# Optimization experiments

Measured on AMD Instinct MI355X. Metric: run time of the kernel, lower is better.

## Reference

```python
import jax, jax.numpy as jnp
import numpy as np

B, S, DIM, HEADS, DHEAD = 1, 1992, 2048, 16, 128
NKI_SEQ_ALIGN = 128
EPS = 1e-6


def setup_inputs() -> dict:
    key = jax.random.key(0)
    ks = jax.random.split(key, 8)
    hidden_states = jax.random.normal(ks[0], (B, S, DIM), dtype=jnp.float32)
    # realistic rotary tables, full head_dim with interleaved pair angles
    pos = jnp.arange(S, dtype=jnp.float32)
    inv_freq = 1.0 / (10000.0 ** (jnp.arange(0, DHEAD, 2, dtype=jnp.float32) / DHEAD))
    ang = pos[:, None] * inv_freq[None, :]                      # [S, DHEAD/2]
    full = jnp.stack([ang, ang], axis=-1).reshape(S, DHEAD)     # interleave
    freqs_cos = jnp.cos(full)[None, :, None, :]                 # [1,S,1,DHEAD]
    freqs_sin = jnp.sin(full)[None, :, None, :]
    sc = 0.02
    wq = jax.random.normal(ks[1], (DIM, DIM), dtype=jnp.float32) * sc
    wk = jax.random.normal(ks[2], (DIM, DIM), dtype=jnp.float32) * sc
    wv = jax.random.normal(ks[3], (DIM, DIM), dtype=jnp.float32) * sc
    wo = jax.random.normal(ks[4], (DIM, DIM), dtype=jnp.float32) * sc
    bq = jax.random.normal(ks[5], (DIM,), dtype=jnp.float32) * sc
    bk = jax.random.normal(ks[6], (DIM,), dtype=jnp.float32) * sc
    bv = jax.random.normal(ks[7], (DIM,), dtype=jnp.float32) * sc
    bo = jnp.zeros((DIM,), dtype=jnp.float32)
    norm_q_w = jnp.ones((DIM,), dtype=jnp.float32)
    norm_k_w = jnp.ones((DIM,), dtype=jnp.float32)
    return dict(hidden_states=hidden_states, freqs_cos=freqs_cos, freqs_sin=freqs_sin,
                wq=wq, bq=bq, wk=wk, bk=bk, wv=wv, bv=bv,
                norm_q_w=norm_q_w, norm_k_w=norm_k_w, wo=wo, bo=bo)


def _rms_norm(x, weight, eps=EPS):
    xf = x.astype(jnp.float32)
    var = jnp.mean(xf * xf, axis=-1, keepdims=True)
    return (weight * (xf * jax.lax.rsqrt(var + eps))).astype(x.dtype)


def _apply_rope(x, freqs_cos, freqs_sin):
    # x: [B,H,S,D]; freqs: [1,S,1,D]
    cos = jnp.transpose(freqs_cos[..., 0::2], (0, 2, 1, 3))  # [1,1,S,D/2]
    sin = jnp.transpose(freqs_sin[..., 1::2], (0, 2, 1, 3))
    x1, x2 = x[..., 0::2], x[..., 1::2]
    o1 = x1 * cos - x2 * sin
    o2 = x1 * sin + x2 * cos
    return jnp.stack([o1, o2], axis=-1).reshape(x.shape)


def _attention_padded(q, k, v):
    # Faithful to nki_flash_attention: zero-pad seq to multiple of 128,
    # no masking of padded keys (they contribute logit 0), trim query pad.
    B_, H_, S_, D_ = q.shape
    pad = (-S_) % NKI_SEQ_ALIGN
    if pad:
        pc = [(0, 0), (0, 0), (0, pad), (0, 0)]
        q = jnp.pad(q, pc); k = jnp.pad(k, pc); v = jnp.pad(v, pc)
    scale = 1.0 / np.sqrt(D_)
    scores = jnp.einsum('bhqd,bhkd->bhqk', q, k) * scale
    probs = jax.nn.softmax(scores, axis=-1)
    out = jnp.einsum('bhqk,bhkd->bhqd', probs, v)
    return out[:, :, :S_, :]


def reference(hidden_states, freqs_cos, freqs_sin, wq, bq, wk, bk, wv, bv,
              norm_q_w, norm_k_w, wo, bo):
    b, s, _ = hidden_states.shape
    q = hidden_states @ wq.T + bq
    k = hidden_states @ wk.T + bk
    v = hidden_states @ wv.T + bv
    q = _rms_norm(q, norm_q_w)
    k = _rms_norm(k, norm_k_w)
    hd = q.shape[-1] // HEADS
    q = q.reshape(b, s, HEADS, hd).transpose(0, 2, 1, 3)
    k = k.reshape(b, s, HEADS, hd).transpose(0, 2, 1, 3)
    v = v.reshape(b, s, HEADS, hd).transpose(0, 2, 1, 3)
    q = _apply_rope(q, freqs_cos, freqs_sin)
    k = _apply_rope(k, freqs_cos, freqs_sin)
    o = _attention_padded(q, k, v)
    o = o.transpose(0, 2, 1, 3).reshape(b, s, -1)
    return o @ wo.T + bo
```

## Files before the change

kernel.cpp:

```cpp
#include <hip/hip_runtime.h>
#include <cstdint>

#define S_REAL 1992
#define S_PAD  2048
#define DIMSZ  2048
#define NHEAD  16
#define DHD    128

typedef float f32x4 __attribute__((ext_vector_type(4)));
typedef __bf16 bf16x8 __attribute__((ext_vector_type(8)));
typedef unsigned short u16x8 __attribute__((ext_vector_type(8)));

__device__ __forceinline__ unsigned short f2bf(float f){
  uint32_t u = __float_as_uint(f);
  u += 0x7fffu + ((u >> 16) & 1u);
  return (unsigned short)(u >> 16);
}

__device__ __forceinline__ void gload16(const void* g, void* l){
  __builtin_amdgcn_global_load_lds(
      (const __attribute__((address_space(1))) uint32_t*)g,
      (__attribute__((address_space(3))) uint32_t*)l,
      16, 0, 0);
}

template<int N> __device__ __forceinline__ void waitbar(){
  if constexpr (N == 8)      asm volatile("s_waitcnt vmcnt(8)\n\ts_barrier" ::: "memory");
  else if constexpr (N == 6) asm volatile("s_waitcnt vmcnt(6)\n\ts_barrier" ::: "memory");
  else if constexpr (N == 4) asm volatile("s_waitcnt vmcnt(4)\n\ts_barrier" ::: "memory");
  else if constexpr (N == 3) asm volatile("s_waitcnt vmcnt(3)\n\ts_barrier" ::: "memory");
  else if constexpr (N == 2) asm volatile("s_waitcnt vmcnt(2)\n\ts_barrier" ::: "memory");
  else                       asm volatile("s_waitcnt vmcnt(0)\n\ts_barrier" ::: "memory");
}

__launch_bounds__(256)
__global__ void k_cvt(const float* __restrict__ src, unsigned short* __restrict__ dst, int n8){
  int i = blockIdx.x * 256 + threadIdx.x;
  if (i >= n8) return;
  const float4* s = (const float4*)src + (size_t)i * 2;
  float4 a = s[0], b = s[1];
  u16x8 o;
  o[0]=f2bf(a.x); o[1]=f2bf(a.y); o[2]=f2bf(a.z); o[3]=f2bf(a.w);
  o[4]=f2bf(b.x); o[5]=f2bf(b.y); o[6]=f2bf(b.z); o[7]=f2bf(b.w);
  *((u16x8*)dst + i) = o;
}

template<int BM, int BN>
__launch_bounds__(512, 2)
__global__ void k_gemm8(const unsigned short* __restrict__ A,
                        const unsigned short* __restrict__ B0,
                        const unsigned short* __restrict__ B1,
                        const unsigned short* __restrict__ B2,
                        const float* __restrict__ bias0,
                        const float* __restrict__ bias1,
                        const float* __restrict__ bias2,
                        float* __restrict__ C0, float* __restrict__ C1, float* __restrict__ C2,
                        int Mreal)
{
  constexpr int WN   = BN / 64;
  constexpr int WM   = 8 / WN;
  constexpr int RM   = BM / WM;
  constexpr int MI   = RM / 16;
  constexpr int NL   = (BM + BN) / 128;
  constexpr int BUFE = (BM + BN) * 32;
  constexpr int BOFF = BM * 32;
  constexpr int NT   = DIMSZ / 32;

  __shared__ unsigned short lds[4 * BUFE];

  const unsigned short* Bm = (blockIdx.z == 0) ? B0 : ((blockIdx.z == 1) ? B1 : B2);
  const float* bias        = (blockIdx.z == 0) ? bias0 : ((blockIdx.z == 1) ? bias1 : bias2);
  float* C                 = (blockIdx.z == 0) ? C0 : ((blockIdx.z == 1) ? C1 : C2);

  const int tid = threadIdx.x;
  const int w = tid >> 6, l = tid & 63;
  const int lr = l & 15, lg = l >> 4;
  const int m0 = blockIdx.x * BM, n0 = blockIdx.y * BN;
  const int wr = (w / WN) * RM, wc = (w % WN) * 64;

  f32x4 acc[MI][4];
  #pragma unroll
  for (int mi = 0; mi < MI; ++mi)
    #pragma unroll
    for (int ni = 0; ni < 4; ++ni)
      acc[mi][ni] = (f32x4){0.f, 0.f, 0.f, 0.f};

#define G8_STAGE(TT) do{                                                          \
    const int k0s = (TT) * 32;                                                    \
    unsigned short* dst = &lds[((TT) & 3) * BUFE];                                \
    _Pragma("unroll")                                                             \
    for (int i_ = 0; i_ < BM / 128; ++i_){                                        \
      int lin = i_ * 512 + tid;                                                   \
      int r_ = lin >> 2, pos_ = lin & 3;                                          \
      int gr_ = m0 + r_; if (gr_ > Mreal - 1) gr_ = Mreal - 1;                    \
      gload16(A + (size_t)gr_ * DIMSZ + k0s + (pos_ ^ ((r_ >> 1) & 3)) * 8,       \
              dst + lin * 8);                                                     \
    }                                                                             \
    _Pragma("unroll")                                                             \
    for (int i_ = 0; i_ < BN / 128; ++i_){                                        \
      int lin = i_ * 512 + tid;                                                   \
      int r_ = lin >> 2, pos_ = lin & 3;                                          \
      gload16(Bm + (size_t)(n0 + r_) * DIMSZ + k0s + (pos_ ^ ((r_ >> 1) & 3)) * 8,\
              dst + BOFF + lin * 8);                                              \
    }                                                                             \
  } while(0)

#define G8_COMPUTE(TT) do{                                                        \
    const unsigned short* sb = &lds[((TT) & 3) * BUFE];                           \
    bf16x8 af_[MI]; bf16x8 bf_[4];                                                \
    _Pragma("unroll")                                                             \
    for (int mi = 0; mi < MI; ++mi){                                              \
      int r_ = wr + mi * 16 + lr;                                                 \
      af_[mi] = *(const bf16x8*)(sb + r_ * 32 + (lg ^ ((r_ >> 1) & 3)) * 8);      \
    }                                                                             \
    _Pragma("unroll")                                                             \
    for (int ni = 0; ni < 4; ++ni){                                               \
      int r_ = wc + ni * 16 + lr;                                                 \
      bf_[ni] = *(const bf16x8*)(sb + BOFF + r_ * 32 + (lg ^ ((r_ >> 1) & 3)) * 8);\
    }                                                                             \
    __builtin_amdgcn_s_setprio(1);                                                \
    _Pragma("unroll")                                                             \
    for (int mi = 0; mi < MI; ++mi)                                               \
      _Pragma("unroll")                                                           \
      for (int ni = 0; ni < 4; ++ni)                                              \
        acc[mi][ni] = __builtin_amdgcn_mfma_f32_16x16x32_bf16(af_[mi], bf_[ni],   \
                                                              acc[mi][ni], 0, 0, 0);\
    __builtin_amdgcn_s_setprio(0);                                                \
  } while(0)

  G8_STAGE(0); G8_STAGE(1); G8_STAGE(2);

  for (int tt = 0; tt < NT - 3; ++tt){
    waitbar<2 * NL>();
    G8_STAGE(tt + 3);
    G8_COMPUTE(tt);
  }
  waitbar<2 * NL>(); G8_COMPUTE(NT - 3);
  waitbar<NL>();     G8_COMPUTE(NT - 2);
  waitbar<0>();      G8_COMPUTE(NT - 1);

#undef G8_STAGE
#undef G8_COMPUTE

  #pragma unroll
  for (int ni = 0; ni < 4; ++ni){
    int col = n0 + wc + ni * 16 + lr;
    float bz = bias[col];
    #pragma unroll
    for (int mi = 0; mi < MI; ++mi){
      #pragma unroll
      for (int j = 0; j < 4; ++j){
        int row = m0 + wr + mi * 16 + lg * 4 + j;
        if (row < Mreal) C[(size_t)row * DIMSZ + col] = acc[mi][ni][j] + bz;
      }
    }
  }
}

__launch_bounds__(256)
__global__ void k_normrope(const float* __restrict__ Xf, const float* __restrict__ nw,
                           const float* __restrict__ fc, const float* __restrict__ fs,
                           unsigned short* __restrict__ Out, float scale, int swz)
{
  const int s = blockIdx.x;
  const int t = threadIdx.x;
  const int w = t >> 6, l = t & 63;
  __shared__ float wred[4];
  float v[8];
  float ss = 0.f;
  if (s < S_REAL){
    const float4* p = (const float4*)(Xf + (size_t)s * DIMSZ) + t * 2;
    float4 a = p[0], b = p[1];
    v[0]=a.x; v[1]=a.y; v[2]=a.z; v[3]=a.w; v[4]=b.x; v[5]=b.y; v[6]=b.z; v[7]=b.w;
    #pragma unroll
    for (int j = 0; j < 8; ++j) ss += v[j] * v[j];
  }
  #pragma unroll
  for (int off = 32; off >= 1; off >>= 1) ss += __shfl_xor(ss, off);
  if (l == 0) wred[w] = ss;
  __syncthreads();
  float tot = wred[0] + wred[1] + wred[2] + wred[3];
  float rinv = rsqrtf(tot * (1.f / DIMSZ) + 1e-6f);

  const int h  = t >> 4;
  const int d0 = (t & 15) * 8;
  const int b  = t & 15;
  const int bsw = swz ? (b ^ (s & 7)) : b;
  unsigned short* dst = Out + ((size_t)h * S_PAD + s) * DHD + bsw * 8;
  u16x8 o;
  if (s < S_REAL){
    #pragma unroll
    for (int i = 0; i < 4; ++i){
      float c_ = fc[s * DHD + d0 + 2 * i];
      float s_ = fs[s * DHD + d0 + 2 * i + 1];
      float x1 = v[2 * i]     * rinv * nw[t * 8 + 2 * i];
      float x2 = v[2 * i + 1] * rinv * nw[t * 8 + 2 * i + 1];
      o[2 * i]     = f2bf((x1 * c_ - x2 * s_) * scale);
      o[2 * i + 1] = f2bf((x1 * s_ + x2 * c_) * scale);
    }
  } else {
    #pragma unroll
    for (int j = 0; j < 8; ++j) o[j] = 0;
  }
  *(u16x8*)dst = o;
}

__launch_bounds__(256)
__global__ void k_vtrans(const float* __restrict__ Vf, unsigned short* __restrict__ Vth)
{
  __shared__ unsigned short tile[64][72];
  const int t = threadIdx.x;
  const int s0 = blockIdx.x * 64, c0 = blockIdx.y * 64;
  #pragma unroll
  for (int i = 0; i < 4; ++i){
    int r = (t >> 4) * 4 + i;
    int s = s0 + r;
    int cq = (t & 15) * 4;
    float4 val = {0.f, 0.f, 0.f, 0.f};
    if (s < S_REAL) val = *((const float4*)(Vf + (size_t)s * DIMSZ + c0) + (t & 15));
    tile[r][cq + 0] = f2bf(val.x);
    tile[r][cq + 1] = f2bf(val.y);
    tile[r][cq + 2] = f2bf(val.z);
    tile[r][cq + 3] = f2bf(val.w);
  }
  __syncthreads();
  const int cl = t >> 2;
  const int cc = c0 + cl;
  #pragma unroll
  for (int bi = 0; bi < 2; ++bi){
    int b = (t & 3) * 2 + bi;
    u16x8 o;
    #pragma unroll
    for (int j = 0; j < 8; ++j) o[j] = tile[b * 8 + j][cl];
    int bsw = b ^ (cc & 7);
    *(u16x8*)(Vth + (size_t)cc * S_PAD + s0 + bsw * 8) = o;
  }
}

__launch_bounds__(256)
__global__ void k_attn(const unsigned short* __restrict__ Qh,
                       const unsigned short* __restrict__ Kh,
                       const unsigned short* __restrict__ Vth,
                       unsigned short* __restrict__ O)
{
  __shared__ unsigned short kbuf[2][64 * 128];
  __shared__ unsigned short vbuf[2][128 * 64];
  __shared__ unsigned short pbuf[4][16 * 64];
  const int h = blockIdx.y;
  const int q0 = blockIdx.x * 64;
  const int t = threadIdx.x, w = t >> 6, l = t & 63;
  const int lr = l & 15, lg = l >> 4;

  const unsigned short* Qp = Qh + ((size_t)h * S_PAD + q0 + w * 16 + lr) * DHD;
  bf16x8 qf[4];
  #pragma unroll
  for (int ks = 0; ks < 4; ++ks) qf[ks] = *(const bf16x8*)(Qp + ks * 32 + lg * 8);

  f32x4 acc[8];
  #pragma unroll
  for (int nf = 0; nf < 8; ++nf) acc[nf] = (f32x4){0.f, 0.f, 0.f, 0.f};
  float m = -3.0e38f, lsum = 0.f;

#define ATT_STAGE(KT, BI) do{                                                       \
    _Pragma("unroll")                                                               \
    for (int i_ = 0; i_ < 4; ++i_){                                                 \
      int rK = (w * 4 + i_) * 4 + (l >> 4);                                         \
      gload16(Kh + ((size_t)h * S_PAD + (KT) * 64 + rK) * DHD + (l & 15) * 8,       \
              &kbuf[BI][(w * 4 + i_) * 512]);                                       \
      int rV = (w * 4 + i_) * 8 + (l >> 3);                                         \
      gload16(Vth + ((size_t)h * DHD + rV) * S_PAD + (KT) * 64 + (l & 7) * 8,       \
              &vbuf[BI][(w * 4 + i_) * 512]);                                       \
    }                                                                               \
  } while(0)

  ATT_STAGE(0, 0);
  __syncthreads();

  for (int kt = 0; kt < S_PAD / 64; ++kt){
    const int bi = kt & 1;
    if (kt < S_PAD / 64 - 1) ATT_STAGE(kt + 1, bi ^ 1);

    f32x4 sf[4];
    __builtin_amdgcn_s_setprio(1);
    #pragma unroll
    for (int kvf = 0; kvf < 4; ++kvf){
      sf[kvf] = (f32x4){0.f, 0.f, 0.f, 0.f};
      int r = kvf * 16 + lr;
      #pragma unroll
      for (int ks = 0; ks < 4; ++ks){
        int blk = (ks * 4 + lg) ^ (r & 7);
        bf16x8 kf = *(const bf16x8*)&kbuf[bi][r * 128 + blk * 8];
        sf[kvf] = __builtin_amdgcn_mfma_f32_16x16x32_bf16(kf, qf[ks], sf[kvf], 0, 0, 0);
      }
    }
    __builtin_amdgcn_s_setprio(0);

    float pmax = sf[0][0];
    #pragma unroll
    for (int kvf = 0; kvf < 4; ++kvf)
      #pragma unroll
      for (int j = 0; j < 4; ++j) pmax = fmaxf(pmax, sf[kvf][j]);
    pmax = fmaxf(pmax, __shfl_xor(pmax, 16));
    pmax = fmaxf(pmax, __shfl_xor(pmax, 32));
    float mn = fmaxf(m, pmax);
    float fr = __expf(m - mn);
    m = mn;
    float p[4][4];
    float psum = 0.f;
    #pragma unroll
    for (int kvf = 0; kvf < 4; ++kvf)
      #pragma unroll
      for (int j = 0; j < 4; ++j){ p[kvf][j] = __expf(sf[kvf][j] - mn); psum += p[kvf][j]; }
    lsum = lsum * fr + psum;

    float fv0 = __shfl(fr, lg * 4 + 0);
    float fv1 = __shfl(fr, lg * 4 + 1);
    float fv2 = __shfl(fr, lg * 4 + 2);
    float fv3 = __shfl(fr, lg * 4 + 3);
    f32x4 fv = (f32x4){fv0, fv1, fv2, fv3};
    #pragma unroll
    for (int nf = 0; nf < 8; ++nf) acc[nf] *= fv;

    char* pb = (char*)pbuf[w];
    #pragma unroll
    for (int kvf = 0; kvf < 4; ++kvf){
      uint2 wv;
      wv.x = (uint32_t)f2bf(p[kvf][0]) | ((uint32_t)f2bf(p[kvf][1]) << 16);
      wv.y = (uint32_t)f2bf(p[kvf][2]) | ((uint32_t)f2bf(p[kvf][3]) << 16);
      int byte = lr * 128 + (((kvf * 2 + (lg >> 1)) ^ (lr & 7)) * 16) + (lg & 1) * 8;
      *(uint2*)(pb + byte) = wv;
    }
    bf16x8 pf[2];
    #pragma unroll
    for (int c = 0; c < 2; ++c)
      pf[c] = *(const bf16x8*)(pb + lr * 128 + ((c * 4 + lg) ^ (lr & 7)) * 16);

    __builtin_amdgcn_s_setprio(1);
    #pragma unroll
    for (int nf = 0; nf < 8; ++nf){
      int cc = nf * 16 + lr;
      #pragma unroll
      for (int ks = 0; ks < 2; ++ks){
        int blk = (ks * 4 + lg) ^ (cc & 7);
        bf16x8 vf = *(const bf16x8*)&vbuf[bi][cc * 64 + blk * 8];
        acc[nf] = __builtin_amdgcn_mfma_f32_16x16x32_bf16(pf[ks], vf, acc[nf], 0, 0, 0);
      }
    }
    __builtin_amdgcn_s_setprio(0);

    __syncthreads();
  }
#undef ATT_STAGE

  lsum += __shfl_xor(lsum, 16);
  lsum += __shfl_xor(lsum, 32);
  float ls0 = __shfl(lsum, lg * 4 + 0);
  float ls1 = __shfl(lsum, lg * 4 + 1);
  float ls2 = __shfl(lsum, lg * 4 + 2);
  float ls3 = __shfl(lsum, lg * 4 + 3);
  f32x4 lsv = (f32x4){1.f / ls0, 1.f / ls1, 1.f / ls2, 1.f / ls3};

  #pragma unroll
  for (int nf = 0; nf < 8; ++nf){
    #pragma unroll
    for (int j = 0; j < 4; ++j){
      int row = q0 + w * 16 + lg * 4 + j;
      if (row < S_REAL)
        O[(size_t)row * DIMSZ + h * DHD + nf * 16 + lr] = f2bf(acc[nf][j] * lsv[j]);
    }
  }
}

extern "C" void kernel_launch(void* const* d_in, const int* in_sizes, int n_in,
                              void* d_out, int out_size, void* d_ws, size_t ws_size,
                              hipStream_t stream)
{
  const float* hidden = (const float*)d_in[0];
  const float* fc  = (const float*)d_in[1];
  const float* fs  = (const float*)d_in[2];
  const float* wq  = (const float*)d_in[3];
  const float* bq  = (const float*)d_in[4];
  const float* wk  = (const float*)d_in[5];
  const float* bk  = (const float*)d_in[6];
  const float* wv  = (const float*)d_in[7];
  const float* bv  = (const float*)d_in[8];
  const float* nqw = (const float*)d_in[9];
  const float* nkw = (const float*)d_in[10];
  const float* wo  = (const float*)d_in[11];
  const float* bo  = (const float*)d_in[12];
  float* out = (float*)d_out;

  char* ws = (char*)d_ws;
  size_t off = 0;
  auto alloc = [&](size_t bytes) -> void* {
    void* p = ws + off;
    off += (bytes + 255) & ~(size_t)255;
    return p;
  };
  unsigned short* Xb  = (unsigned short*)alloc((size_t)S_REAL * DIMSZ * 2);
  unsigned short* Wqb = (unsigned short*)alloc((size_t)DIMSZ * DIMSZ * 2);
  unsigned short* Wkb = (unsigned short*)alloc((size_t)DIMSZ * DIMSZ * 2);
  unsigned short* Wvb = (unsigned short*)alloc((size_t)DIMSZ * DIMSZ * 2);
  unsigned short* Wob = (unsigned short*)alloc((size_t)DIMSZ * DIMSZ * 2);
  float* Qf = (float*)alloc((size_t)S_REAL * DIMSZ * 4);
  float* Kf = (float*)alloc((size_t)S_REAL * DIMSZ * 4);
  float* Vf = (float*)alloc((size_t)S_REAL * DIMSZ * 4);
  unsigned short* Qhh = (unsigned short*)alloc((size_t)NHEAD * S_PAD * DHD * 2);
  unsigned short* Khh = (unsigned short*)alloc((size_t)NHEAD * S_PAD * DHD * 2);
  unsigned short* Vth = (unsigned short*)alloc((size_t)NHEAD * DHD * S_PAD * 2);
  unsigned short* Oa  = (unsigned short*)alloc((size_t)S_REAL * DIMSZ * 2);

  k_cvt<<<S_REAL * DIMSZ / 8 / 256, 256, 0, stream>>>(hidden, Xb, S_REAL * DIMSZ / 8);
  k_cvt<<<DIMSZ * DIMSZ / 8 / 256, 256, 0, stream>>>(wq, Wqb, DIMSZ * DIMSZ / 8);
  k_cvt<<<DIMSZ * DIMSZ / 8 / 256, 256, 0, stream>>>(wk, Wkb, DIMSZ * DIMSZ / 8);
  k_cvt<<<DIMSZ * DIMSZ / 8 / 256, 256, 0, stream>>>(wv, Wvb, DIMSZ * DIMSZ / 8);
  k_cvt<<<DIMSZ * DIMSZ / 8 / 256, 256, 0, stream>>>(wo, Wob, DIMSZ * DIMSZ / 8);

  k_gemm8<256, 256><<<dim3(8, 8, 3), 512, 0, stream>>>(Xb, Wqb, Wkb, Wvb, bq, bk, bv,
                                                       Qf, Kf, Vf, S_REAL);

  k_normrope<<<S_PAD, 256, 0, stream>>>(Qf, nqw, fc, fs, Qhh, 0.08838834764831843f, 0);
  k_normrope<<<S_PAD, 256, 0, stream>>>(Kf, nkw, fc, fs, Khh, 1.0f, 1);

  k_vtrans<<<dim3(S_PAD / 64, DIMSZ / 64), 256, 0, stream>>>(Vf, Vth);

  k_attn<<<dim3(S_PAD / 64, NHEAD), 256, 0, stream>>>(Qhh, Khh, Vth, Oa);

  k_gemm8<128, 128><<<dim3(16, 16, 1), 512, 0, stream>>>(Oa, Wob, Wob, Wob, bo, bo, bo,
                                                         out, out, out, S_REAL);
}
```

Measured before the change: 218.6 us.

## Merge conversion and norm-rope launches, retile GEMMs to 256 threads with XCD swizzle

Replaces the five bf16 conversion launches with one combined kernel and the two norm+rope launches with one 2D-grid launch, cutting launch count. The GEMM moves to 4 waves per block: QKV uses 128x128 tiles over 768 blocks instead of 256x256 over 192, and the output projection uses 128x64 tiles. A block-id remap spreads consecutive tiles across the 8 XCDs. Smaller tiles give more parallelism but less data reuse per block.

```diff
diff --git a/kernel.cpp b/kernel.cpp
--- a/kernel.cpp
+++ b/kernel.cpp
@@ -34,20 +34,34 @@
 }
 
 __launch_bounds__(256)
-__global__ void k_cvt(const float* __restrict__ src, unsigned short* __restrict__ dst, int n8){
+__global__ void k_cvt5(const float* __restrict__ s0, const float* __restrict__ s1,
+                       const float* __restrict__ s2, const float* __restrict__ s3,
+                       const float* __restrict__ s4,
+                       unsigned short* __restrict__ d0, unsigned short* __restrict__ d1,
+                       unsigned short* __restrict__ d2, unsigned short* __restrict__ d3,
+                       unsigned short* __restrict__ d4,
+                       int nX, int nW)
+{
   int i = blockIdx.x * 256 + threadIdx.x;
-  if (i >= n8) return;
-  const float4* s = (const float4*)src + (size_t)i * 2;
-  float4 a = s[0], b = s[1];
+  const float* s; unsigned short* d; int j;
+  if (i < nX){ s = s0; d = d0; j = i; }
+  else {
+    int k = i - nX;
+    int wsel = k / nW; j = k - wsel * nW;
+    s = (wsel == 0) ? s1 : (wsel == 1) ? s2 : (wsel == 2) ? s3 : s4;
+    d = (wsel == 0) ? d1 : (wsel == 1) ? d2 : (wsel == 2) ? d3 : d4;
+  }
+  const float4* sp = (const float4*)s + (size_t)j * 2;
+  float4 a = sp[0], b = sp[1];
   u16x8 o;
   o[0]=f2bf(a.x); o[1]=f2bf(a.y); o[2]=f2bf(a.z); o[3]=f2bf(a.w);
   o[4]=f2bf(b.x); o[5]=f2bf(b.y); o[6]=f2bf(b.z); o[7]=f2bf(b.w);
-  *((u16x8*)dst + i) = o;
+  *((u16x8*)d + j) = o;
 }
 
 template<int BM, int BN>
-__launch_bounds__(512, 2)
-__global__ void k_gemm8(const unsigned short* __restrict__ A,
+__launch_bounds__(256, 2)
+__global__ void k_gemm4(const unsigned short* __restrict__ A,
                         const unsigned short* __restrict__ B0,
                         const unsigned short* __restrict__ B1,
                         const unsigned short* __restrict__ B2,
@@ -57,14 +71,17 @@
                         float* __restrict__ C0, float* __restrict__ C1, float* __restrict__ C2,
                         int Mreal)
 {
+  constexpr int AR   = BM / 64;
+  constexpr int BR   = BN / 64;
+  constexpr int NL   = AR + BR;
   constexpr int WN   = BN / 64;
-  constexpr int WM   = 8 / WN;
+  constexpr int WM   = 4 / WN;
   constexpr int RM   = BM / WM;
   constexpr int MI   = RM / 16;
-  constexpr int NL   = (BM + BN) / 128;
   constexpr int BUFE = (BM + BN) * 32;
   constexpr int BOFF = BM * 32;
   constexpr int NT   = DIMSZ / 32;
+  constexpr int TN   = DIMSZ / BN;
 
   __shared__ unsigned short lds[4 * BUFE];
 
@@ -72,10 +89,14 @@
   const float* bias        = (blockIdx.z == 0) ? bias0 : ((blockIdx.z == 1) ? bias1 : bias2);
   float* C                 = (blockIdx.z == 0) ? C0 : ((blockIdx.z == 1) ? C1 : C2);
 
+  const int fid = blockIdx.x + gridDim.x * blockIdx.y;
+  const int q   = (gridDim.x * gridDim.y) >> 3;
+  const int nf  = (fid & 7) * q + (fid >> 3);
+  const int m0  = (nf / TN) * BM, n0 = (nf % TN) * BN;
+
   const int tid = threadIdx.x;
   const int w = tid >> 6, l = tid & 63;
   const int lr = l & 15, lg = l >> 4;
-  const int m0 = blockIdx.x * BM, n0 = blockIdx.y * BN;
   const int wr = (w / WN) * RM, wc = (w % WN) * 64;
 
   f32x4 acc[MI][4];
@@ -89,16 +110,16 @@
     const int k0s = (TT) * 32;                                                    \
     unsigned short* dst = &lds[((TT) & 3) * BUFE];                                \
     _Pragma("unroll")                                                             \
-    for (int i_ = 0; i_ < BM / 128; ++i_){                                        \
-      int lin = i_ * 512 + tid;                                                   \
+    for (int i_ = 0; i_ < AR; ++i_){                                              \
+      int lin = i_ * 256 + tid;                                                   \
       int r_ = lin >> 2, pos_ = lin & 3;                                          \
       int gr_ = m0 + r_; if (gr_ > Mreal - 1) gr_ = Mreal - 1;                    \
       gload16(A + (size_t)gr_ * DIMSZ + k0s + (pos_ ^ ((r_ >> 1) & 3)) * 8,       \
               dst + lin * 8);                                                     \
     }                                                                             \
     _Pragma("unroll")                                                             \
-    for (int i_ = 0; i_ < BN / 128; ++i_){                                        \
-      int lin = i_ * 512 + tid;                                                   \
+    for (int i_ = 0; i_ < BR; ++i_){                                              \
+      int lin = i_ * 256 + tid;                                                   \
       int r_ = lin >> 2, pos_ = lin & 3;                                          \
       gload16(Bm + (size_t)(n0 + r_) * DIMSZ + k0s + (pos_ ^ ((r_ >> 1) & 3)) * 8,\
               dst + BOFF + lin * 8);                                              \
@@ -158,11 +179,19 @@
 }
 
 __launch_bounds__(256)
-__global__ void k_normrope(const float* __restrict__ Xf, const float* __restrict__ nw,
-                           const float* __restrict__ fc, const float* __restrict__ fs,
-                           unsigned short* __restrict__ Out, float scale, int swz)
+__global__ void k_normrope2(const float* __restrict__ Qf, const float* __restrict__ Kf,
+                            const float* __restrict__ nqw, const float* __restrict__ nkw,
+                            const float* __restrict__ fc, const float* __restrict__ fs,
+                            unsigned short* __restrict__ OutQ, unsigned short* __restrict__ OutK)
 {
   const int s = blockIdx.x;
+  const int isK = blockIdx.y;
+  const float* Xf = isK ? Kf : Qf;
+  const float* nw = isK ? nkw : nqw;
+  unsigned short* Out = isK ? OutK : OutQ;
+  const float scale = isK ? 1.0f : 0.08838834764831843f;
+  const int swz = isK;
+
   const int t = threadIdx.x;
   const int w = t >> 6, l = t & 63;
   __shared__ float wred[4];
@@ -410,22 +439,23 @@
   unsigned short* Vth = (unsigned short*)alloc((size_t)NHEAD * DHD * S_PAD * 2);
   unsigned short* Oa  = (unsigned short*)alloc((size_t)S_REAL * DIMSZ * 2);
 
-  k_cvt<<<S_REAL * DIMSZ / 8 / 256, 256, 0, stream>>>(hidden, Xb, S_REAL * DIMSZ / 8);
-  k_cvt<<<DIMSZ * DIMSZ / 8 / 256, 256, 0, stream>>>(wq, Wqb, DIMSZ * DIMSZ / 8);
-  k_cvt<<<DIMSZ * DIMSZ / 8 / 256, 256, 0, stream>>>(wk, Wkb, DIMSZ * DIMSZ / 8);
-  k_cvt<<<DIMSZ * DIMSZ / 8 / 256, 256, 0, stream>>>(wv, Wvb, DIMSZ * DIMSZ / 8);
-  k_cvt<<<DIMSZ * DIMSZ / 8 / 256, 256, 0, stream>>>(wo, Wob, DIMSZ * DIMSZ / 8);
-
-  k_gemm8<256, 256><<<dim3(8, 8, 3), 512, 0, stream>>>(Xb, Wqb, Wkb, Wvb, bq, bk, bv,
-                                                       Qf, Kf, Vf, S_REAL);
-
-  k_normrope<<<S_PAD, 256, 0, stream>>>(Qf, nqw, fc, fs, Qhh, 0.08838834764831843f, 0);
-  k_normrope<<<S_PAD, 256, 0, stream>>>(Kf, nkw, fc, fs, Khh, 1.0f, 1);
+  {
+    int nX = S_REAL * DIMSZ / 8;
+    int nW = DIMSZ * DIMSZ / 8;
+    int total = nX + 4 * nW;
+    k_cvt5<<<total / 256, 256, 0, stream>>>(hidden, wq, wk, wv, wo,
+                                            Xb, Wqb, Wkb, Wvb, Wob, nX, nW);
+  }
+
+  k_gemm4<128, 128><<<dim3(16, 16, 3), 256, 0, stream>>>(Xb, Wqb, Wkb, Wvb, bq, bk, bv,
+                                                         Qf, Kf, Vf, S_REAL);
+
+  k_normrope2<<<dim3(S_PAD, 2), 256, 0, stream>>>(Qf, Kf, nqw, nkw, fc, fs, Qhh, Khh);
 
   k_vtrans<<<dim3(S_PAD / 64, DIMSZ / 64), 256, 0, stream>>>(Vf, Vth);
 
   k_attn<<<dim3(S_PAD / 64, NHEAD), 256, 0, stream>>>(Qhh, Khh, Vth, Oa);
 
-  k_gemm8<128, 128><<<dim3(16, 16, 1), 512, 0, stream>>>(Oa, Wob, Wob, Wob, bo, bo, bo,
-                                                         out, out, out, S_REAL);
-}
+  k_gemm4<128, 64><<<dim3(16, 32, 1), 256, 0, stream>>>(Oa, Wob, Wob, Wob, bo, bo, bo,
+                                                        out, out, out, S_REAL);
+}
```

After: 221.8 us. About the same (+1.5%).
